# Optimization experiments

Hardware: AMD Instinct MI355X
Metric: run time of the kernel (lower is better)

The kernel has to match this reference:

```python
import jax, jax.numpy as jnp
import numpy as np

N_NODES = 100000
N_EDGES = 1600000
IN_FEATS = 128
HEADS = 4
OUT_FEATS = 16
NEG_SLOPE = 0.2  # DGL GATConv default negative_slope


def setup_inputs() -> dict:
    key = jax.random.key(0)
    ks = jax.random.split(key, 7)
    feats = jax.random.normal(ks[0], (N_NODES, IN_FEATS), dtype=jnp.float32)
    W = jax.random.normal(ks[1], (HEADS * OUT_FEATS, IN_FEATS), dtype=jnp.float32) * 0.05
    attn_l = jax.random.normal(ks[2], (HEADS, OUT_FEATS), dtype=jnp.float32) * 0.1
    attn_r = jax.random.normal(ks[3], (HEADS, OUT_FEATS), dtype=jnp.float32) * 0.1
    bias = jax.random.normal(ks[4], (HEADS * OUT_FEATS,), dtype=jnp.float32) * 0.01
    src = jax.random.randint(ks[5], (N_EDGES,), 0, N_NODES, dtype=jnp.int64 if jax.config.jax_enable_x64 else jnp.int32)
    dst = jax.random.randint(ks[6], (N_EDGES,), 0, N_NODES, dtype=jnp.int64 if jax.config.jax_enable_x64 else jnp.int32)
    return {"feats": feats, "W": W, "attn_l": attn_l, "attn_r": attn_r,
            "bias": bias, "src": src, "dst": dst}


def reference(feats, W, attn_l, attn_r, bias, src, dst):
    """GATConv forward on a homogeneous graph built from concatenated edge lists.

    feats: [N, in_feats]; W: [H*F, in_feats]; attn_l/attn_r: [H, F]; bias: [H*F]
    src/dst: [E] edge endpoint indices. Returns [N, H, F] (DGL GATConv output).
    """
    N = feats.shape[0]
    H, F = attn_l.shape
    # Linear projection, per-head split: z [N, H, F]
    z = (feats @ W.T).reshape(N, H, F)
    # Per-node attention logits: el/er [N, H]
    el = jnp.einsum('nhf,hf->nh', z, attn_l)
    er = jnp.einsum('nhf,hf->nh', z, attn_r)
    # Per-edge unnormalized attention: e [E, H]
    e = jax.nn.leaky_relu(el[src] + er[dst], negative_slope=NEG_SLOPE)
    # Edge softmax over incoming edges of each destination node
    m = jax.ops.segment_max(e, dst, num_segments=N)           # [N, H]
    m = jnp.where(jnp.isfinite(m), m, jnp.zeros_like(m))      # guard empty segments
    ex = jnp.exp(e - m[dst])                                  # [E, H]
    denom = jax.ops.segment_sum(ex, dst, num_segments=N)      # [N, H]
    alpha = ex / denom[dst]                                   # [E, H]
    # Weighted message aggregation: scatter-add z[src] * alpha into dst
    msg = z[src] * alpha[:, :, None]                          # [E, H, F]
    out = jax.ops.segment_sum(msg, dst, num_segments=N)       # [N, H, F]
    return out + bias.reshape(1, H, F)
```

## Files before the change

### kernel.cpp

```cpp
#include <hip/hip_runtime.h>

#define N_NODES 100000
#define N_EDGES 1600000
#define IN_F    128
#define HEADS   4
#define OUT_F   16
#define HF      64
#define NEG_SLOPE 0.2f

#define BUCK    112
#define NBUCK   893
#define BSTRIDE 2048
#define BSC_CHUNK 3072
#define NB_BSC  522

#define NB_MFMA2 782
#define NB_FUSED2 1305

typedef __attribute__((ext_vector_type(8))) short short8;
typedef __attribute__((ext_vector_type(4))) float f32x4;

__device__ __forceinline__ short f2bf(float f) {
    union { float f; unsigned u; } v; v.f = f;
    return (short)((v.u + 0x7FFFu + ((v.u >> 16) & 1u)) >> 16);
}

__global__ __launch_bounds__(256) void k_prep(const float* __restrict__ W,
                                              const float* __restrict__ attn_l,
                                              const float* __restrict__ attn_r,
                                              unsigned short* __restrict__ Wfrag,
                                              int* __restrict__ gcur) {
    const int g = blockIdx.x, t = threadIdx.x;
    if (g >= 20) {
        int i = (g - 20) * 256 + t;
        if (i < 1024) gcur[i] = 0;
        return;
    }
    const int ct = g >> 2, kf = g & 3;
    #pragma unroll
    for (int e = 0; e < 2; ++e) {
        int off = e * 256 + t;
        int j = off & 7, lane = off >> 3;
        int n = lane & 15, qq = lane >> 4;
        int k = kf * 32 + qq * 8 + j;
        float v;
        if (ct < 4) {
            v = W[(size_t)(ct * 16 + n) * IN_F + k];
        } else if (n < 8) {
            int hh = n & 3;
            const float* at = (n < 4) ? attn_l : attn_r;
            v = 0.f;
            #pragma unroll
            for (int f = 0; f < 16; ++f)
                v += W[(size_t)(hh * 16 + f) * IN_F + k] * at[hh * 16 + f];
        } else {
            v = 0.f;
        }
        Wfrag[(size_t)g * 512 + off] = (unsigned short)f2bf(v);
    }
}

__global__ __launch_bounds__(512) void k_fused(const float* __restrict__ feats,
                                               const unsigned short* __restrict__ Wfrag,
                                               unsigned short* __restrict__ zb,
                                               float* __restrict__ el,
                                               float* __restrict__ er,
                                               const int* __restrict__ src,
                                               const int* __restrict__ dst,
                                               int* __restrict__ gcur,
                                               unsigned* __restrict__ bin) {
    const unsigned bx = blockIdx.x;
    const unsigned q5 = bx / 5u, r5 = bx % 5u;
    const int t = threadIdx.x;

    if (r5 < 2u) {
        const int bid = (int)(q5 * 2u + r5);
        const int start = bid * BSC_CHUNK;
        if (start >= N_EDGES) return;
        __shared__ int h[NBUCK], cur[NBUCK];
        for (int i = t; i < NBUCK; i += 512) h[i] = 0;
        __syncthreads();
        int end = start + BSC_CHUNK;
        if (end > N_EDGES) end = N_EDGES;

        int myd[6];
        #pragma unroll
        for (int k = 0; k < 6; ++k) {
            int i = start + t + k * 512;
            myd[k] = (i < end) ? dst[i] : -1;
            if (myd[k] >= 0) atomicAdd(&h[(unsigned)myd[k] / BUCK], 1);
        }
        __syncthreads();
        for (int i = t; i < NBUCK; i += 512) cur[i] = h[i] ? atomicAdd(&gcur[i], h[i]) : 0;
        __syncthreads();
        #pragma unroll
        for (int k = 0; k < 6; ++k) {
            int i = start + t + k * 512;
            if (i < end) {
                unsigned d = (unsigned)myd[k];
                unsigned b = d / BUCK;
                unsigned dl = d - b * BUCK;
                int pos = atomicAdd(&cur[b], 1);
                if (pos < BSTRIDE)
                    bin[(size_t)b * BSTRIDE + pos] = (unsigned)src[i] | (dl << 17);
            }
        }
        return;
    }

    const int bid = (int)(q5 * 3u + (r5 - 2u));
    if (bid >= NB_MFMA2) return;

    const int grp = t >> 6;
    const int l = t & 63;
    const int q = l >> 4, n = l & 15;

    short8 bfrag[5][4];
    #pragma unroll
    for (int ct = 0; ct < 5; ++ct)
        #pragma unroll
        for (int kf = 0; kf < 4; ++kf)
            bfrag[ct][kf] = *(const short8*)(Wfrag + (size_t)((ct * 4 + kf) * 64 + l) * 8);

    int anode = bid * 128 + grp * 16 + n;
    int aclamp = anode < N_NODES ? anode : 0;
    const float* arow = feats + (size_t)aclamp * IN_F + q * 8;

    f32x4 acc[5];
    #pragma unroll
    for (int ct = 0; ct < 5; ++ct) acc[ct] = (f32x4){0.f, 0.f, 0.f, 0.f};

    #pragma unroll
    for (int kf = 0; kf < 4; ++kf) {
        float4 x = *(const float4*)(arow + kf * 32);
        float4 y = *(const float4*)(arow + kf * 32 + 4);
        short8 a;
        a[0] = f2bf(x.x); a[1] = f2bf(x.y); a[2] = f2bf(x.z); a[3] = f2bf(x.w);
        a[4] = f2bf(y.x); a[5] = f2bf(y.y); a[6] = f2bf(y.z); a[7] = f2bf(y.w);
        #pragma unroll
        for (int ct = 0; ct < 5; ++ct)
            acc[ct] = __builtin_amdgcn_mfma_f32_16x16x32_bf16(a, bfrag[ct][kf], acc[ct], 0, 0, 0);
    }

    #pragma unroll
    for (int reg = 0; reg < 4; ++reg) {
        int onode = bid * 128 + grp * 16 + q * 4 + reg;
        if (onode >= N_NODES) continue;
        #pragma unroll
        for (int ct = 0; ct < 4; ++ct)
            zb[(size_t)onode * HF + ct * 16 + n] = (unsigned short)f2bf(acc[ct][reg]);
        float v4 = acc[4][reg];
        if (n < 4)       el[onode * HEADS + n] = v4;
        else if (n < 8)  er[onode * HEADS + (n - 4)] = v4;
    }
}

__global__ __launch_bounds__(512) void k3_sort(const unsigned* __restrict__ bin,
                                               const int* __restrict__ gcur,
                                               const float* __restrict__ el,
                                               const float* __restrict__ er,
                                               const unsigned short* __restrict__ zb,
                                               const float* __restrict__ bias,
                                               float* __restrict__ out) {
    __shared__ unsigned raw[BSTRIDE];
    __shared__ unsigned sorted[BSTRIDE];
    __shared__ int hist[BUCK];
    __shared__ int noff[BUCK + 1];
    __shared__ int cur[BUCK];
    __shared__ int s[128];
    __shared__ float er_s[BUCK * HEADS];

    const int t = threadIdx.x;
    const int B = blockIdx.x;
    const int nodebase = B * BUCK;
    const unsigned* mybin = bin + (size_t)B * BSTRIDE;
    int cnt = gcur[B];
    if (cnt > BSTRIDE) cnt = BSTRIDE;

    if (t < BUCK) hist[t] = 0;
    if (t < BUCK * HEADS) {
        int g = nodebase * HEADS + t;
        er_s[t] = (g < N_NODES * HEADS) ? er[g] : 0.f;
    }
    for (int i = t; i < cnt; i += 512) raw[i] = mybin[i];
    __syncthreads();

    for (int i = t; i < cnt; i += 512)
        atomicAdd(&hist[raw[i] >> 17], 1);
    __syncthreads();

    if (t < 128) s[t] = (t < BUCK) ? hist[t] : 0;
    __syncthreads();
    for (int o = 1; o < 128; o <<= 1) {
        int x = (t < 128 && t >= o) ? s[t - o] : 0;
        __syncthreads();
        if (t < 128) s[t] += x;
        __syncthreads();
    }
    if (t < BUCK) {
        int excl = s[t] - hist[t];
        noff[t] = excl;
        cur[t] = excl;
    }
    if (t == 0) noff[BUCK] = s[BUCK - 1];
    __syncthreads();

    for (int i = t; i < cnt; i += 512) {
        unsigned p = raw[i];
        int pos = atomicAdd(&cur[p >> 17], 1);
        sorted[pos] = p & 0x1FFFF;
    }
    __syncthreads();

    const int wave = t >> 6, lane = t & 63;
    const int j = lane >> 3;
    const int c = lane & 7;
    const int h = c >> 1;
    const int jj = j & 3;
    const int sel = j >> 2;

    for (int p = wave; p < BUCK / 2; p += 8) {
        const int nl = p * 2 + sel;
        const int node = nodebase + nl;
        const int nlo = noff[nl], nhi = noff[nl + 1];
        const float er_d = er_s[nl * HEADS + h];

        float4 A0 = make_float4(0.f, 0.f, 0.f, 0.f);
        float4 A1 = make_float4(0.f, 0.f, 0.f, 0.f);
        float den = 0.f;
        for (int i = nlo + jj; i < nhi; i += 4) {
            int sN = (int)sorted[i];
            float x = el[sN * HEADS + h] + er_d;
            x = x > 0.f ? x : NEG_SLOPE * x;
            float ex = __expf(x);
            den += ex;
            uint4 v = *(const uint4*)(zb + (size_t)sN * HF + c * 8);
            A0.x += ex * __uint_as_float(v.x << 16);
            A0.y += ex * __uint_as_float(v.x & 0xFFFF0000u);
            A0.z += ex * __uint_as_float(v.y << 16);
            A0.w += ex * __uint_as_float(v.y & 0xFFFF0000u);
            A1.x += ex * __uint_as_float(v.z << 16);
            A1.y += ex * __uint_as_float(v.z & 0xFFFF0000u);
            A1.z += ex * __uint_as_float(v.w << 16);
            A1.w += ex * __uint_as_float(v.w & 0xFFFF0000u);
        }
        #pragma unroll
        for (int m = 8; m <= 16; m <<= 1) {
            A0.x += __shfl_xor(A0.x, m); A0.y += __shfl_xor(A0.y, m);
            A0.z += __shfl_xor(A0.z, m); A0.w += __shfl_xor(A0.w, m);
            A1.x += __shfl_xor(A1.x, m); A1.y += __shfl_xor(A1.y, m);
            A1.z += __shfl_xor(A1.z, m); A1.w += __shfl_xor(A1.w, m);
            den  += __shfl_xor(den,  m);
        }
        if (jj == 0 && node < N_NODES) {
            float4 b0 = *(const float4*)(bias + c * 8);
            float4 b1 = *(const float4*)(bias + c * 8 + 4);
            if (den > 0.f) {
                float inv = 1.f / den;
                b0.x += A0.x * inv; b0.y += A0.y * inv;
                b0.z += A0.z * inv; b0.w += A0.w * inv;
                b1.x += A1.x * inv; b1.y += A1.y * inv;
                b1.z += A1.z * inv; b1.w += A1.w * inv;
            }
            *(float4*)(out + (size_t)node * HF + c * 8) = b0;
            *(float4*)(out + (size_t)node * HF + c * 8 + 4) = b1;
        }
    }
}

extern "C" void kernel_launch(void* const* d_in, const int* in_sizes, int n_in,
                              void* d_out, int out_size, void* d_ws, size_t ws_size,
                              hipStream_t stream) {
    const float* feats  = (const float*)d_in[0];
    const float* W      = (const float*)d_in[1];
    const float* attn_l = (const float*)d_in[2];
    const float* attn_r = (const float*)d_in[3];
    const float* bias   = (const float*)d_in[4];
    const int*   src    = (const int*)d_in[5];
    const int*   dst    = (const int*)d_in[6];
    float* out = (float*)d_out;

    char* ws = (char*)d_ws;
    unsigned short* zb = (unsigned short*)ws;  ws += (size_t)N_NODES * HF * 2;
    float* el    = (float*)ws;                 ws += N_NODES * HEADS * 4;
    float* er    = (float*)ws;                 ws += N_NODES * HEADS * 4;
    unsigned short* Wfrag = (unsigned short*)ws; ws += 20 * 64 * 8 * 2;
    int*   gcur  = (int*)ws;                   ws += 1024 * 4;
    unsigned* bin = (unsigned*)ws;             ws += (size_t)NBUCK * BSTRIDE * 4;

    k_prep  <<<24,         256,  0, stream>>>(W, attn_l, attn_r, Wfrag, gcur);
    k_fused <<<NB_FUSED2,  512,  0, stream>>>(feats, Wfrag, zb, el, er, src, dst, gcur, bin);
    k3_sort <<<NBUCK,      512,  0, stream>>>(bin, gcur, el, er, zb, bias, out);
}
```

Before: 175.0 us.

## Locally sort edge chunks in LDS before writing to global buckets

The binning blocks now each take a much larger 16K-edge chunk. Each block histograms destinations into buckets, prefix-scans the histogram, and scatters the packed edges into a shared-memory staging array grouped by bucket. Each bucket's run is then copied to its global bin slot in one pass, so writes are grouped per bucket instead of scattered to random addresses, and far fewer global atomics on gcur are needed. The interleaved 2:3 block split is replaced with a simple split: all binning blocks come first, followed by the MFMA blocks. The tradeoffs are fewer, heavier binning blocks, serialized per-thread copy loops for each bucket (so stores are not coalesced across threads), and 64KB+ of LDS per block, which limits occupancy.

```diff
diff --git a/kernel.cpp b/kernel.cpp
--- a/kernel.cpp
+++ b/kernel.cpp
@@ -11,11 +11,12 @@
 #define BUCK    112
 #define NBUCK   893
 #define BSTRIDE 2048
-#define BSC_CHUNK 3072
-#define NB_BSC  522
+
+#define BSC_CHUNK 16384
+#define NB_BSC3 98
 
 #define NB_MFMA2 782
-#define NB_FUSED2 1305
+#define NB_FUSED3 880
 
 typedef __attribute__((ext_vector_type(8))) short short8;
 typedef __attribute__((ext_vector_type(4))) float f32x4;
@@ -69,47 +70,78 @@
                                                const int* __restrict__ dst,
                                                int* __restrict__ gcur,
                                                unsigned* __restrict__ bin) {
-    const unsigned bx = blockIdx.x;
-    const unsigned q5 = bx / 5u, r5 = bx % 5u;
     const int t = threadIdx.x;
 
-    if (r5 < 2u) {
-        const int bid = (int)(q5 * 2u + r5);
+    if (blockIdx.x < NB_BSC3) {
+        __shared__ unsigned sortedL[BSC_CHUNK];
+        __shared__ int hist[NBUCK];
+        __shared__ int noff[NBUCK];
+        __shared__ int cur[NBUCK];
+        __shared__ int gbase[NBUCK];
+
+        const int bid = blockIdx.x;
         const int start = bid * BSC_CHUNK;
-        if (start >= N_EDGES) return;
-        __shared__ int h[NBUCK], cur[NBUCK];
-        for (int i = t; i < NBUCK; i += 512) h[i] = 0;
-        __syncthreads();
         int end = start + BSC_CHUNK;
         if (end > N_EDGES) end = N_EDGES;
 
-        int myd[6];
-        #pragma unroll
-        for (int k = 0; k < 6; ++k) {
-            int i = start + t + k * 512;
-            myd[k] = (i < end) ? dst[i] : -1;
-            if (myd[k] >= 0) atomicAdd(&h[(unsigned)myd[k] / BUCK], 1);
-        }
-        __syncthreads();
-        for (int i = t; i < NBUCK; i += 512) cur[i] = h[i] ? atomicAdd(&gcur[i], h[i]) : 0;
-        __syncthreads();
-        #pragma unroll
-        for (int k = 0; k < 6; ++k) {
-            int i = start + t + k * 512;
-            if (i < end) {
-                unsigned d = (unsigned)myd[k];
-                unsigned b = d / BUCK;
-                unsigned dl = d - b * BUCK;
-                int pos = atomicAdd(&cur[b], 1);
-                if (pos < BSTRIDE)
-                    bin[(size_t)b * BSTRIDE + pos] = (unsigned)src[i] | (dl << 17);
+        for (int i = t; i < NBUCK; i += 512) hist[i] = 0;
+        __syncthreads();
+
+        for (int i = start + t; i < end; i += 512)
+            atomicAdd(&hist[(unsigned)dst[i] / BUCK], 1);
+        __syncthreads();
+
+        if (t < 64) {
+            int base = t * 14;
+            int loc[14]; int acc = 0;
+            #pragma unroll
+            for (int k = 0; k < 14; ++k) {
+                int idx = base + k;
+                int v = (idx < NBUCK) ? hist[idx] : 0;
+                loc[k] = acc; acc += v;
+            }
+            int x = acc;
+            #pragma unroll
+            for (int o = 1; o < 64; o <<= 1) {
+                int y = __shfl_up(x, o);
+                if (t >= o) x += y;
+            }
+            int excl = x - acc;
+            #pragma unroll
+            for (int k = 0; k < 14; ++k) {
+                int idx = base + k;
+                if (idx < NBUCK) noff[idx] = excl + loc[k];
+            }
+        }
+        __syncthreads();
+
+        for (int b = t; b < NBUCK; b += 512) {
+            cur[b] = noff[b];
+            gbase[b] = hist[b] ? atomicAdd(&gcur[b], hist[b]) : 0;
+        }
+        __syncthreads();
+
+        for (int i = start + t; i < end; i += 512) {
+            unsigned d = (unsigned)dst[i];
+            unsigned b = d / BUCK;
+            unsigned dl = d - b * BUCK;
+            int pos = atomicAdd(&cur[b], 1);
+            sortedL[pos] = (unsigned)src[i] | (dl << 17);
+        }
+        __syncthreads();
+
+        for (int b = t; b < NBUCK; b += 512) {
+            int n = hist[b], lo = noff[b], gb = gbase[b];
+            unsigned* dp = bin + (size_t)b * BSTRIDE;
+            for (int k2 = 0; k2 < n; ++k2) {
+                int gpos = gb + k2;
+                if (gpos < BSTRIDE) dp[gpos] = sortedL[lo + k2];
             }
         }
         return;
     }
 
-    const int bid = (int)(q5 * 3u + (r5 - 2u));
-    if (bid >= NB_MFMA2) return;
+    const int bid = (int)blockIdx.x - NB_BSC3;
 
     const int grp = t >> 6;
     const int l = t & 63;
@@ -289,6 +321,6 @@
     unsigned* bin = (unsigned*)ws;             ws += (size_t)NBUCK * BSTRIDE * 4;
 
     k_prep  <<<24,         256,  0, stream>>>(W, attn_l, attn_r, Wfrag, gcur);
-    k_fused <<<NB_FUSED2,  512,  0, stream>>>(feats, Wfrag, zb, el, er, src, dst, gcur, bin);
+    k_fused <<<NB_FUSED3,  512,  0, stream>>>(feats, Wfrag, zb, el, er, src, dst, gcur, bin);
     k3_sort <<<NBUCK,      512,  0, stream>>>(bin, gcur, el, er, zb, bias, out);
 }
```

New measurement: 189.5 us. 1.08x slower.
